# Optimization experiments

Hardware: AMD Instinct MI355X
Metric: run time of the kernel (lower is better)

Reference implementation:

```python
import jax, jax.numpy as jnp
import numpy as np

N, E, D_IN, H, D_OUT = 50000, 1600000, 256, 128, 64


def setup_inputs() -> dict:
    key = jax.random.key(0)
    ks = jax.random.split(key, 8)
    x = jax.random.normal(ks[0], (N, D_IN), dtype=jnp.float32)
    edge_index = jax.random.randint(ks[1], (2, E), 0, N, dtype=jnp.int64)
    W1 = jax.random.normal(ks[2], (D_IN, H), dtype=jnp.float32) / np.float32(np.sqrt(D_IN))
    b1 = jnp.zeros((H,), jnp.float32)
    W2 = jax.random.normal(ks[3], (H, H), dtype=jnp.float32) / np.float32(np.sqrt(H))
    b2 = jnp.zeros((H,), jnp.float32)
    W3 = jax.random.normal(ks[4], (H, D_OUT), dtype=jnp.float32) / np.float32(np.sqrt(H))
    b3 = jnp.zeros((D_OUT,), jnp.float32)
    return {"x": x, "W1": W1, "b1": b1, "W2": W2, "b2": b2, "W3": W3, "b3": b3,
            "edge_index": edge_index}


def reference(x, W1, b1, W2, b2, W3, b3, edge_index):
    n = x.shape[0]
    # GCN: add self-loops, symmetric normalization D^{-1/2}(A+I)D^{-1/2}
    loop = jnp.arange(n, dtype=edge_index.dtype)
    src = jnp.concatenate([edge_index[0], loop])
    dst = jnp.concatenate([edge_index[1], loop])
    deg = jax.ops.segment_sum(jnp.ones_like(dst, x.dtype), dst, num_segments=n)
    dinv = jnp.where(deg > 0, jax.lax.rsqrt(deg), 0.0).astype(x.dtype)
    norm = dinv[src] * dinv[dst]  # [E+N]

    def gcn_layer(h, W, b):
        h = h @ W                                   # [N, F_out]
        msg = norm[:, None] * h[src]                # gather + scale, [E+N, F_out]
        return jax.ops.segment_sum(msg, dst, num_segments=n) + b

    h = jax.nn.relu(gcn_layer(x, W1, b1))
    h = jax.nn.relu(gcn_layer(h, W2, b2))
    return gcn_layer(h, W3, b3)
```

## Files before the change

kernel.cpp:

```cpp
#include <hip/hip_runtime.h>


constexpr int DIN = 256;
constexpr int HID = 128;
constexpr int DOUT = 64;
constexpr int MAXB = 1024;
constexpr int BSH = 6;
constexpr int EPB = 8192;

typedef unsigned short ushort_t;
typedef unsigned int uint_t;
typedef __attribute__((ext_vector_type(8))) short bf16x8;
typedef __attribute__((ext_vector_type(4))) float f32x4;

__device__ inline ushort_t f2bf(float f) {
  uint_t u = __float_as_uint(f);
  u += 0x7FFF + ((u >> 16) & 1);
  return (ushort_t)(u >> 16);
}
__device__ inline float bf2f(ushort_t b) {
  return __uint_as_float(((uint_t)b) << 16);
}

template <int SH>
__device__ inline uint_t ldrow32(const ushort_t* __restrict__ t, int c, uint_t lb) {
  return *(const uint_t*)((const char*)t + ((((uint_t)c) << SH) | lb));
}
template <int SH>
__device__ inline ushort_t ldrow16(const ushort_t* __restrict__ t, int c, uint_t lb) {
  return *(const ushort_t*)((const char*)t + ((((uint_t)c) << SH) | lb));
}
__device__ inline float ldf32(const float* __restrict__ p, int c) {
  return *(const float*)((const char*)p + (((uint_t)c) << 2));
}


__device__ inline void wprep_one(const float* __restrict__ W, ushort_t* __restrict__ Bhi,
                                 ushort_t* __restrict__ Blo, int K, int F, int i) {
  int k = i / F, nn = i % F;
  int t = nn >> 4, s = k >> 5, q = (k >> 3) & 3, j = k & 7;
  int lane = q * 16 + (nn & 15);
  int KS = K >> 5;
  size_t idx = (((size_t)t * KS + s) * 64 + (size_t)lane) * 8 + j;
  float w = W[i];
  ushort_t h = f2bf(w);
  float r = w - bf2f(h);
  Bhi[idx] = h;
  Blo[idx] = f2bf(r);
}


__global__ __launch_bounds__(256) void initprep_kernel(
    int* __restrict__ bucket_total, int* __restrict__ done, int iblocks,
    const float* __restrict__ W1, ushort_t* __restrict__ W1hi, ushort_t* __restrict__ W1lo,
    const float* __restrict__ W2, ushort_t* __restrict__ W2hi, ushort_t* __restrict__ W2lo,
    const float* __restrict__ W3, ushort_t* __restrict__ W3hi, ushort_t* __restrict__ W3lo) {
  if ((int)blockIdx.x < iblocks) {
    int i = blockIdx.x * 256 + threadIdx.x;
    if (i < MAXB) bucket_total[i] = 0;
    if (i == 0) *done = 0;
  } else {
    int idx = ((int)blockIdx.x - iblocks) * 256 + threadIdx.x;
    constexpr int S1 = DIN * HID;
    constexpr int S2 = S1 + HID * HID;
    constexpr int S3 = S2 + HID * DOUT;
    if (idx < S1) wprep_one(W1, W1hi, W1lo, DIN, HID, idx);
    else if (idx < S2) wprep_one(W2, W2hi, W2lo, HID, HID, idx - S1);
    else if (idx < S3) wprep_one(W3, W3hi, W3lo, HID, DOUT, idx - S2);
  }
}


__global__ __launch_bounds__(256) void bin_kernel(const int* __restrict__ dst, int e,
    int nbuckets, int* __restrict__ bucket_total, int* __restrict__ block_base,
    int* __restrict__ bucket_base, int* __restrict__ done, int nbin) {
  __shared__ int h[MAXB];
  __shared__ int lastflag;
  int tid = threadIdx.x;
  for (int i = tid; i < nbuckets; i += 256) h[i] = 0;
  __syncthreads();
  int base = blockIdx.x * EPB;
  int end = min(base + EPB, e);
  for (int i = base + tid; i < end; i += 256) atomicAdd(&h[dst[i] >> BSH], 1);
  __syncthreads();
  for (int i = tid; i < nbuckets; i += 256) {
    int v = h[i];
    if (v) block_base[(size_t)blockIdx.x * nbuckets + i] = atomicAdd(&bucket_total[i], v);
  }
  __threadfence();
  __syncthreads();
  if (tid == 0) lastflag = (atomicAdd(done, 1) == nbin - 1) ? 1 : 0;
  __syncthreads();
  if (!lastflag) return;
  int a[4];
  int ls = 0;
#pragma unroll
  for (int k = 0; k < 4; ++k) {
    int idx = tid * 4 + k;
    a[k] = (idx < nbuckets) ? atomicAdd(&bucket_total[idx], 0) : 0;
    ls += a[k];
  }
  __syncthreads();
  h[tid] = ls;
  __syncthreads();
  for (int off = 1; off < 256; off <<= 1) {
    int u = (tid >= off) ? h[tid - off] : 0;
    __syncthreads();
    h[tid] += u;
    __syncthreads();
  }
  int run = h[tid] - ls;
#pragma unroll
  for (int k = 0; k < 4; ++k) {
    int idx = tid * 4 + k;
    if (idx < nbuckets) bucket_base[idx] = run;
    run += a[k];
  }
  if (tid == 255) bucket_base[nbuckets] = h[255];
}


template <int K, int F, bool SCALE>
__device__ inline void gemm_mfma_dev(const float* __restrict__ X,
    const ushort_t* __restrict__ Bhi, const ushort_t* __restrict__ Blo,
    const float* __restrict__ dinv, ushort_t* __restrict__ T, int n, int bid) {
  constexpr int NT = F / 16;
  constexpr int KS = K / 32;
  int wave = threadIdx.x >> 6;
  int lane = threadIdx.x & 63;
  int q = lane >> 4;
  int m = lane & 15;
  int arow = bid * 64 + wave * 16 + m;
  bool valid = arow < n;
  const float* xrow = X + (size_t)arow * K;

  f32x4 acc[NT];
#pragma unroll
  for (int t = 0; t < NT; ++t) acc[t] = (f32x4){0.f, 0.f, 0.f, 0.f};

  for (int s = 0; s < KS; ++s) {
    float av[8];
    if (valid) {
      float4 u0 = *(const float4*)(xrow + s * 32 + q * 8);
      float4 u1 = *(const float4*)(xrow + s * 32 + q * 8 + 4);
      av[0] = u0.x; av[1] = u0.y; av[2] = u0.z; av[3] = u0.w;
      av[4] = u1.x; av[5] = u1.y; av[6] = u1.z; av[7] = u1.w;
    } else {
#pragma unroll
      for (int j = 0; j < 8; ++j) av[j] = 0.f;
    }
    bf16x8 ahi, alo;
#pragma unroll
    for (int j = 0; j < 8; ++j) {
      ushort_t h = f2bf(av[j]);
      ahi[j] = (short)h;
      alo[j] = (short)f2bf(av[j] - bf2f(h));
    }
#pragma unroll
    for (int t = 0; t < NT; ++t) {
      size_t boff = (((size_t)t * KS + s) * 64 + (size_t)lane) * 8;
      bf16x8 bh = *(const bf16x8*)(Bhi + boff);
      bf16x8 bl = *(const bf16x8*)(Blo + boff);
      acc[t] = __builtin_amdgcn_mfma_f32_16x16x32_bf16(ahi, bh, acc[t], 0, 0, 0);
      acc[t] = __builtin_amdgcn_mfma_f32_16x16x32_bf16(alo, bh, acc[t], 0, 0, 0);
      acc[t] = __builtin_amdgcn_mfma_f32_16x16x32_bf16(ahi, bl, acc[t], 0, 0, 0);
    }
  }

  int orow_base = bid * 64 + wave * 16 + q * 4;
#pragma unroll
  for (int r = 0; r < 4; ++r) {
    int orow = orow_base + r;
    if (orow >= n) continue;
    float sc = SCALE ? dinv[orow] : 1.0f;
    ushort_t* trow = T + (size_t)orow * F + m;
#pragma unroll
    for (int t = 0; t < NT; ++t) trow[t * 16] = f2bf(sc * acc[t][r]);
  }
}


__global__ __launch_bounds__(256) void fusedA2_kernel(
    const float* __restrict__ X, const ushort_t* __restrict__ Bhi,
    const ushort_t* __restrict__ Blo, ushort_t* __restrict__ T, int n, int gblocks,
    const int* __restrict__ src, const int* __restrict__ dst,
    const int* __restrict__ bucket_base, const int* __restrict__ block_base,
    uint_t* __restrict__ binned, int e, int nbuckets) {
  if ((int)blockIdx.x < gblocks) {
    gemm_mfma_dev<DIN, HID, false>(X, Bhi, Blo, nullptr, T, n, blockIdx.x);
  } else {
    __shared__ int rkh[MAXB];
    __shared__ int cbase[MAXB];
    int tid = threadIdx.x;
    int blk = (int)blockIdx.x - gblocks;
    for (int i = tid; i < nbuckets; i += 256) {
      rkh[i] = 0;
      cbase[i] = bucket_base[i] + block_base[(size_t)blk * nbuckets + i];
    }
    __syncthreads();
    int base = blk * EPB;
    int end = min(base + EPB, e);
    for (int i = base + tid; i < end; i += 256) {
      int d = dst[i];
      int s = src[i];
      int b = d >> BSH;
      int r = atomicAdd(&rkh[b], 1);
      binned[cbase[b] + r] = ((uint_t)d << 16) | (uint_t)s;
    }
  }
}


__global__ __launch_bounds__(256) void csr_kernel(const uint_t* __restrict__ binned,
    const int* __restrict__ bucket_base, int n, int* __restrict__ row_start,
    int* __restrict__ deg, float* __restrict__ dinv, int* __restrict__ col) {
  __shared__ int cnt[64];
  __shared__ int rk[64];
  __shared__ int rs[64];
  __shared__ int ebs[2];
  int tid = threadIdx.x;
  int b = blockIdx.x;
  int node0 = b << BSH;
  if (tid < 64) { cnt[tid] = 0; rk[tid] = 0; }
  if (tid == 0) { ebs[0] = bucket_base[b]; ebs[1] = bucket_base[b + 1]; }
  __syncthreads();
  int ebase = ebs[0];
  int esz = ebs[1] - ebase;
  for (int i = tid; i < esz; i += 256)
    atomicAdd(&cnt[(int)(binned[ebase + i] >> 16) - node0], 1);
  __syncthreads();
  if (tid < 64) {
    int v = cnt[tid];
    int inc = v;
#pragma unroll
    for (int off = 1; off < 64; off <<= 1) {
      int u = __shfl_up(inc, off, 64);
      if (tid >= off) inc += u;
    }
    rs[tid] = inc - v;
    int node = node0 + tid;
    if (node < n) {
      deg[node] = v + 1;
      dinv[node] = rsqrtf((float)(v + 1));
      row_start[node] = ebase + (inc - v);
    }
  }
  __syncthreads();
  for (int i = tid; i < esz; i += 256) {
    uint_t p = binned[ebase + i];
    int l = (int)(p >> 16) - node0;
    int r = atomicAdd(&rk[l], 1);
    col[ebase + rs[l] + r] = (int)(p & 0xFFFFu);
  }
}


template <int FOUT, bool GD>
__global__ __launch_bounds__(256) void spmm_gemm_kernel(
    const ushort_t* __restrict__ t, const int* __restrict__ row_start,
    const int* __restrict__ deg, const int* __restrict__ col,
    const float* __restrict__ dinv, const float* __restrict__ bias,
    const ushort_t* __restrict__ Bhi, const ushort_t* __restrict__ Blo,
    ushort_t* __restrict__ Tout, int n) {
  constexpr int FIN = 128;
  constexpr int NPB = 8;
  constexpr int LDW = FIN + 4;
  __shared__ float agg[16][LDW];
  int wave = threadIdx.x >> 6;
  int lane = threadIdx.x & 63;
  int tid = threadIdx.x;
  int nb0 = (int)blockIdx.x * NPB;
  uint_t lb = (uint_t)lane << 2;

  {
    float* z = &agg[8][0];
    for (int i = tid; i < 8 * LDW; i += 256) z[i] = 0.f;
  }

  {
    int ln0 = wave * 2;
    int n0 = nb0 + ln0;
    int n1 = n0 + 1;
    bool h0 = n0 < n, h1 = n1 < n;
    int rs0 = h0 ? row_start[n0] : 0, e0 = h0 ? deg[n0] - 1 : 0;
    int rs1 = h1 ? row_start[n1] : 0, e1 = h1 ? deg[n1] - 1 : 0;
    float di0 = h0 ? dinv[n0] : 0.f;
    float di1 = h1 ? dinv[n1] : 0.f;
    float bx = bias[2 * lane], by = bias[2 * lane + 1];
    float ax0 = 0.f, ay0 = 0.f, ax1 = 0.f, ay1 = 0.f;
    if (h0) {
      uint_t s0 = ldrow32<8>(t, n0, lb);
      ax0 = bf2f((ushort_t)(s0 & 0xFFFF)); ay0 = bf2f((ushort_t)(s0 >> 16));
      if constexpr (GD) { ax0 *= di0; ay0 *= di0; }
    }
    if (h1) {
      uint_t s1 = ldrow32<8>(t, n1, lb);
      ax1 = bf2f((ushort_t)(s1 & 0xFFFF)); ay1 = bf2f((ushort_t)(s1 >> 16));
      if constexpr (GD) { ax1 *= di1; ay1 *= di1; }
    }
    int p0 = rs0, q0 = rs0 + e0;
    int p1 = rs1, q1 = rs1 + e1;
    while (p0 + 4 <= q0 && p1 + 4 <= q1) {
      int c[8];
      uint_t v[8];
      float dc[8];
#pragma unroll
      for (int j = 0; j < 4; ++j) { c[j] = col[p0 + j]; c[4 + j] = col[p1 + j]; }
#pragma unroll
      for (int j = 0; j < 8; ++j) {
        v[j] = ldrow32<8>(t, c[j], lb);
        if constexpr (GD) dc[j] = ldf32(dinv, c[j]);
      }
#pragma unroll
      for (int j = 0; j < 4; ++j) {
        if constexpr (GD) {
          ax0 = fmaf(dc[j], bf2f((ushort_t)(v[j] & 0xFFFF)), ax0);
          ay0 = fmaf(dc[j], bf2f((ushort_t)(v[j] >> 16)), ay0);
          ax1 = fmaf(dc[4 + j], bf2f((ushort_t)(v[4 + j] & 0xFFFF)), ax1);
          ay1 = fmaf(dc[4 + j], bf2f((ushort_t)(v[4 + j] >> 16)), ay1);
        } else {
          ax0 += bf2f((ushort_t)(v[j] & 0xFFFF));
          ay0 += bf2f((ushort_t)(v[j] >> 16));
          ax1 += bf2f((ushort_t)(v[4 + j] & 0xFFFF));
          ay1 += bf2f((ushort_t)(v[4 + j] >> 16));
        }
      }
      p0 += 4; p1 += 4;
    }
    for (; p0 + 4 <= q0; p0 += 4) {
      int c[4]; uint_t v[4]; float dc[4];
#pragma unroll
      for (int j = 0; j < 4; ++j) c[j] = col[p0 + j];
#pragma unroll
      for (int j = 0; j < 4; ++j) {
        v[j] = ldrow32<8>(t, c[j], lb);
        if constexpr (GD) dc[j] = ldf32(dinv, c[j]);
      }
#pragma unroll
      for (int j = 0; j < 4; ++j) {
        if constexpr (GD) {
          ax0 = fmaf(dc[j], bf2f((ushort_t)(v[j] & 0xFFFF)), ax0);
          ay0 = fmaf(dc[j], bf2f((ushort_t)(v[j] >> 16)), ay0);
        } else {
          ax0 += bf2f((ushort_t)(v[j] & 0xFFFF)); ay0 += bf2f((ushort_t)(v[j] >> 16));
        }
      }
    }
    for (; p0 < q0; ++p0) {
      int c = col[p0];
      uint_t v = ldrow32<8>(t, c, lb);
      if constexpr (GD) {
        float d = ldf32(dinv, c);
        ax0 = fmaf(d, bf2f((ushort_t)(v & 0xFFFF)), ax0);
        ay0 = fmaf(d, bf2f((ushort_t)(v >> 16)), ay0);
      } else {
        ax0 += bf2f((ushort_t)(v & 0xFFFF)); ay0 += bf2f((ushort_t)(v >> 16));
      }
    }
    for (; p1 + 4 <= q1; p1 += 4) {
      int c[4]; uint_t v[4]; float dc[4];
#pragma unroll
      for (int j = 0; j < 4; ++j) c[j] = col[p1 + j];
#pragma unroll
      for (int j = 0; j < 4; ++j) {
        v[j] = ldrow32<8>(t, c[j], lb);
        if constexpr (GD) dc[j] = ldf32(dinv, c[j]);
      }
#pragma unroll
      for (int j = 0; j < 4; ++j) {
        if constexpr (GD) {
          ax1 = fmaf(dc[j], bf2f((ushort_t)(v[j] & 0xFFFF)), ax1);
          ay1 = fmaf(dc[j], bf2f((ushort_t)(v[j] >> 16)), ay1);
        } else {
          ax1 += bf2f((ushort_t)(v[j] & 0xFFFF)); ay1 += bf2f((ushort_t)(v[j] >> 16));
        }
      }
    }
    for (; p1 < q1; ++p1) {
      int c = col[p1];
      uint_t v = ldrow32<8>(t, c, lb);
      if constexpr (GD) {
        float d = ldf32(dinv, c);
        ax1 = fmaf(d, bf2f((ushort_t)(v & 0xFFFF)), ax1);
        ay1 = fmaf(d, bf2f((ushort_t)(v >> 16)), ay1);
      } else {
        ax1 += bf2f((ushort_t)(v & 0xFFFF)); ay1 += bf2f((ushort_t)(v >> 16));
      }
    }
    float2 o0, o1;
    o0.x = h0 ? fmaxf(fmaf(di0, ax0, bx), 0.f) : 0.f;
    o0.y = h0 ? fmaxf(fmaf(di0, ay0, by), 0.f) : 0.f;
    o1.x = h1 ? fmaxf(fmaf(di1, ax1, bx), 0.f) : 0.f;
    o1.y = h1 ? fmaxf(fmaf(di1, ay1, by), 0.f) : 0.f;
    *(float2*)&agg[ln0][2 * lane] = o0;
    *(float2*)&agg[ln0 + 1][2 * lane] = o1;
  }
  __syncthreads();

  constexpr int NT = FOUT / 16;
  constexpr int KS = FIN / 32;
  constexpr int NTW = NT / 4;
  int q = lane >> 4, m = lane & 15;
  f32x4 acc[NTW];
#pragma unroll
  for (int tt = 0; tt < NTW; ++tt) acc[tt] = (f32x4){0.f, 0.f, 0.f, 0.f};
  const float* arow = &agg[m][0];
#pragma unroll
  for (int s = 0; s < KS; ++s) {
    float4 u0 = *(const float4*)(arow + s * 32 + q * 8);
    float4 u1 = *(const float4*)(arow + s * 32 + q * 8 + 4);
    float av[8];
    av[0] = u0.x; av[1] = u0.y; av[2] = u0.z; av[3] = u0.w;
    av[4] = u1.x; av[5] = u1.y; av[6] = u1.z; av[7] = u1.w;
    bf16x8 ahi, alo;
#pragma unroll
    for (int j = 0; j < 8; ++j) {
      ushort_t h = f2bf(av[j]);
      ahi[j] = (short)h;
      alo[j] = (short)f2bf(av[j] - bf2f(h));
    }
#pragma unroll
    for (int tt = 0; tt < NTW; ++tt) {
      int tg = wave * NTW + tt;
      size_t boff = (((size_t)tg * KS + s) * 64 + (size_t)lane) * 8;
      bf16x8 bh = *(const bf16x8*)(Bhi + boff);
      bf16x8 bl = *(const bf16x8*)(Blo + boff);
      acc[tt] = __builtin_amdgcn_mfma_f32_16x16x32_bf16(ahi, bh, acc[tt], 0, 0, 0);
      acc[tt] = __builtin_amdgcn_mfma_f32_16x16x32_bf16(alo, bh, acc[tt], 0, 0, 0);
      acc[tt] = __builtin_amdgcn_mfma_f32_16x16x32_bf16(ahi, bl, acc[tt], 0, 0, 0);
    }
  }
#pragma unroll
  for (int r = 0; r < 4; ++r) {
    int row = q * 4 + r;
    if (row >= NPB) continue;
    int orow = nb0 + row;
    if (orow >= n) continue;
    float sc = dinv[orow];
    ushort_t* trow = Tout + (size_t)orow * FOUT + m;
#pragma unroll
    for (int tt = 0; tt < NTW; ++tt)
      trow[(wave * NTW + tt) * 16] = f2bf(sc * acc[tt][r]);
  }
}


template <int F, bool RELU>
__global__ __launch_bounds__(256) void spmm_kernel(const ushort_t* __restrict__ t,
    const int* __restrict__ row_start, const int* __restrict__ deg,
    const int* __restrict__ col, const float* __restrict__ dinv,
    const float* __restrict__ bias, float* __restrict__ out, int n) {
  static_assert(F == 64, "final layer only");
  int gw = (int)((blockIdx.x * 256u + threadIdx.x) >> 6);
  int lane = threadIdx.x & 63;
  int n0 = gw * 2;
  int n1 = n0 + 1;
  if (n0 >= n) return;
  bool h1 = (n1 < n);
  int rs0 = row_start[n0], e0 = deg[n0] - 1;
  int rs1 = h1 ? row_start[n1] : 0, e1 = h1 ? (deg[n1] - 1) : 0;
  float di0 = dinv[n0];
  float di1 = h1 ? dinv[n1] : 0.f;
  uint_t lb = (uint_t)lane << 1;

  float a0 = bf2f(ldrow16<7>(t, n0, lb));
  float a1 = h1 ? bf2f(ldrow16<7>(t, n1, lb)) : 0.f;
  int p0 = rs0, q0 = rs0 + e0;
  int p1 = rs1, q1 = rs1 + e1;
  while (p0 + 4 <= q0 && p1 + 4 <= q1) {
    int c[8];
    ushort_t v[8];
#pragma unroll
    for (int j = 0; j < 4; ++j) { c[j] = col[p0 + j]; c[4 + j] = col[p1 + j]; }
#pragma unroll
    for (int j = 0; j < 8; ++j) v[j] = ldrow16<7>(t, c[j], lb);
#pragma unroll
    for (int j = 0; j < 4; ++j) { a0 += bf2f(v[j]); a1 += bf2f(v[4 + j]); }
    p0 += 4; p1 += 4;
  }
  for (; p0 + 4 <= q0; p0 += 4) {
    int c[4]; ushort_t v[4];
#pragma unroll
    for (int j = 0; j < 4; ++j) c[j] = col[p0 + j];
#pragma unroll
    for (int j = 0; j < 4; ++j) v[j] = ldrow16<7>(t, c[j], lb);
#pragma unroll
    for (int j = 0; j < 4; ++j) a0 += bf2f(v[j]);
  }
  for (; p0 < q0; ++p0) a0 += bf2f(ldrow16<7>(t, col[p0], lb));
  for (; p1 + 4 <= q1; p1 += 4) {
    int c[4]; ushort_t v[4];
#pragma unroll
    for (int j = 0; j < 4; ++j) c[j] = col[p1 + j];
#pragma unroll
    for (int j = 0; j < 4; ++j) v[j] = ldrow16<7>(t, c[j], lb);
#pragma unroll
    for (int j = 0; j < 4; ++j) a1 += bf2f(v[j]);
  }
  for (; p1 < q1; ++p1) a1 += bf2f(ldrow16<7>(t, col[p1], lb));
  float b = bias[lane];
  a0 = fmaf(di0, a0, b);
  if constexpr (RELU) a0 = fmaxf(a0, 0.f);
  out[(size_t)n0 * F + lane] = a0;
  if (h1) {
    a1 = fmaf(di1, a1, b);
    if constexpr (RELU) a1 = fmaxf(a1, 0.f);
    out[(size_t)n1 * F + lane] = a1;
  }
}


extern "C" void kernel_launch(void* const* d_in, const int* in_sizes, int n_in,
                              void* d_out, int out_size, void* d_ws, size_t ws_size,
                              hipStream_t stream) {
  const float* x  = (const float*)d_in[0];
  const float* W1 = (const float*)d_in[1];
  const float* b1 = (const float*)d_in[2];
  const float* W2 = (const float*)d_in[3];
  const float* b2 = (const float*)d_in[4];
  const float* W3 = (const float*)d_in[5];
  const float* b3 = (const float*)d_in[6];
  const int* ei   = (const int*)d_in[7];

  int n = in_sizes[0] / DIN;
  int e = in_sizes[7] / 2;
  const int* src = ei;
  const int* dst = ei + e;

  char* ws = (char*)d_ws;
  size_t off = 0;
  auto alloc = [&](size_t bytes) -> void* {
    off = (off + 255) & ~(size_t)255;
    void* p = ws + off;
    off += bytes;
    return p;
  };
  int nbuckets = (n + 63) >> BSH;
  int nbin = (e + EPB - 1) / EPB;

  int*      bucket_total = (int*)alloc((size_t)MAXB * 4);
  int*      bucket_base  = (int*)alloc((size_t)(MAXB + 1) * 4);
  int*      done         = (int*)alloc(256);
  int*      block_base   = (int*)alloc((size_t)nbin * nbuckets * 4);
  uint_t*   binned       = (uint_t*)alloc((size_t)e * 4);
  int*      deg          = (int*)alloc((size_t)n * 4);
  float*    dinv         = (float*)alloc((size_t)n * 4);
  int*      row_start    = (int*)alloc((size_t)n * 4);
  int*      col          = (int*)alloc((size_t)e * 4);
  ushort_t* Ta           = (ushort_t*)alloc((size_t)n * HID * 2);
  ushort_t* Tb           = (ushort_t*)alloc((size_t)n * HID * 2);
  ushort_t* W1hi         = (ushort_t*)alloc((size_t)DIN * HID * 2);
  ushort_t* W1lo         = (ushort_t*)alloc((size_t)DIN * HID * 2);
  ushort_t* W2hi         = (ushort_t*)alloc((size_t)HID * HID * 2);
  ushort_t* W2lo         = (ushort_t*)alloc((size_t)HID * HID * 2);
  ushort_t* W3hi         = (ushort_t*)alloc((size_t)HID * DOUT * 2);
  ushort_t* W3lo         = (ushort_t*)alloc((size_t)HID * DOUT * 2);
  (void)ws_size;

  int gemm_blocks = (n + 63) / 64;
  int sg_blocks = (n + 7) / 8;
  int nwaves = (n + 1) / 2;
  int spmm_blocks = (nwaves + 3) / 4;
  constexpr int WPREP_TOTAL = DIN * HID + HID * HID + HID * DOUT;
  int wblocks = (WPREP_TOTAL + 255) / 256;
  int iblocks = MAXB / 256;

  initprep_kernel<<<iblocks + wblocks, 256, 0, stream>>>(
      bucket_total, done, iblocks,
      W1, W1hi, W1lo, W2, W2hi, W2lo, W3, W3hi, W3lo);
  bin_kernel<<<nbin, 256, 0, stream>>>(dst, e, nbuckets, bucket_total, block_base,
                                       bucket_base, done, nbin);
  fusedA2_kernel<<<gemm_blocks + nbin, 256, 0, stream>>>(
      x, W1hi, W1lo, Ta, n, gemm_blocks,
      src, dst, bucket_base, block_base, binned, e, nbuckets);
  csr_kernel<<<nbuckets, 256, 0, stream>>>(binned, bucket_base, n, row_start, deg, dinv, col);

  spmm_gemm_kernel<HID, true><<<sg_blocks, 256, 0, stream>>>(
      Ta, row_start, deg, col, dinv, b1, W2hi, W2lo, Tb, n);
  spmm_gemm_kernel<DOUT, false><<<sg_blocks, 256, 0, stream>>>(
      Tb, row_start, deg, col, dinv, b2, W3hi, W3lo, Ta, n);
  spmm_kernel<DOUT, false><<<spmm_blocks, 256, 0, stream>>>(
      Ta, row_start, deg, col, dinv, b3, (float*)d_out, n);
}
```

Baseline: 361.8 us.

## Split bucket scan into own kernel and remap final SpMM to half-wave per node

Removes the last-block-done atomic counter and threadfence from the binning kernel and moves the bucket prefix scan into a separate single-block kernel. The final 64-wide SpMM now gives each half-wave one node, with each lane loading two bf16 features as a 32-bit word and writing float2 outputs. Both nodes in a wave step through the longer edge list together with predicated loads. The changes cut global synchronisation and per-lane load count, at the price of one extra launch and lanes that sit idle when the two nodes have unequal degrees.

```diff
diff --git a/kernel.cpp b/kernel.cpp
--- a/kernel.cpp
+++ b/kernel.cpp
@@ -25,10 +25,6 @@
 template <int SH>
 __device__ inline uint_t ldrow32(const ushort_t* __restrict__ t, int c, uint_t lb) {
   return *(const uint_t*)((const char*)t + ((((uint_t)c) << SH) | lb));
-}
-template <int SH>
-__device__ inline ushort_t ldrow16(const ushort_t* __restrict__ t, int c, uint_t lb) {
-  return *(const ushort_t*)((const char*)t + ((((uint_t)c) << SH) | lb));
 }
 __device__ inline float ldf32(const float* __restrict__ p, int c) {
   return *(const float*)((const char*)p + (((uint_t)c) << 2));
@@ -51,14 +47,13 @@
 
 
 __global__ __launch_bounds__(256) void initprep_kernel(
-    int* __restrict__ bucket_total, int* __restrict__ done, int iblocks,
+    int* __restrict__ bucket_total, int iblocks,
     const float* __restrict__ W1, ushort_t* __restrict__ W1hi, ushort_t* __restrict__ W1lo,
     const float* __restrict__ W2, ushort_t* __restrict__ W2hi, ushort_t* __restrict__ W2lo,
     const float* __restrict__ W3, ushort_t* __restrict__ W3hi, ushort_t* __restrict__ W3lo) {
   if ((int)blockIdx.x < iblocks) {
     int i = blockIdx.x * 256 + threadIdx.x;
     if (i < MAXB) bucket_total[i] = 0;
-    if (i == 0) *done = 0;
   } else {
     int idx = ((int)blockIdx.x - iblocks) * 256 + threadIdx.x;
     constexpr int S1 = DIN * HID;
@@ -72,10 +67,8 @@
 
 
 __global__ __launch_bounds__(256) void bin_kernel(const int* __restrict__ dst, int e,
-    int nbuckets, int* __restrict__ bucket_total, int* __restrict__ block_base,
-    int* __restrict__ bucket_base, int* __restrict__ done, int nbin) {
+    int nbuckets, int* __restrict__ bucket_total, int* __restrict__ block_base) {
   __shared__ int h[MAXB];
-  __shared__ int lastflag;
   int tid = threadIdx.x;
   for (int i = tid; i < nbuckets; i += 256) h[i] = 0;
   __syncthreads();
@@ -87,36 +80,37 @@
     int v = h[i];
     if (v) block_base[(size_t)blockIdx.x * nbuckets + i] = atomicAdd(&bucket_total[i], v);
   }
-  __threadfence();
-  __syncthreads();
-  if (tid == 0) lastflag = (atomicAdd(done, 1) == nbin - 1) ? 1 : 0;
-  __syncthreads();
-  if (!lastflag) return;
+}
+
+
+__global__ __launch_bounds__(256) void scan_buckets_kernel(const int* __restrict__ total,
+    int* __restrict__ base, int nb) {
+  __shared__ int sums[256];
+  int t = threadIdx.x;
   int a[4];
   int ls = 0;
 #pragma unroll
   for (int k = 0; k < 4; ++k) {
-    int idx = tid * 4 + k;
-    a[k] = (idx < nbuckets) ? atomicAdd(&bucket_total[idx], 0) : 0;
+    int idx = t * 4 + k;
+    a[k] = (idx < nb) ? total[idx] : 0;
     ls += a[k];
   }
-  __syncthreads();
-  h[tid] = ls;
+  sums[t] = ls;
   __syncthreads();
   for (int off = 1; off < 256; off <<= 1) {
-    int u = (tid >= off) ? h[tid - off] : 0;
+    int u = (t >= off) ? sums[t - off] : 0;
     __syncthreads();
-    h[tid] += u;
+    sums[t] += u;
     __syncthreads();
   }
-  int run = h[tid] - ls;
+  int run = sums[t] - ls;
 #pragma unroll
   for (int k = 0; k < 4; ++k) {
-    int idx = tid * 4 + k;
-    if (idx < nbuckets) bucket_base[idx] = run;
+    int idx = t * 4 + k;
+    if (idx < nb) base[idx] = run;
     run += a[k];
   }
-  if (tid == 255) bucket_base[nbuckets] = h[255];
+  if (t == 255) base[nb] = sums[255];
 }
 
 
@@ -445,67 +439,55 @@
 }
 
 
-template <int F, bool RELU>
-__global__ __launch_bounds__(256) void spmm_kernel(const ushort_t* __restrict__ t,
+__global__ __launch_bounds__(256) void spmm64_kernel(const ushort_t* __restrict__ t,
     const int* __restrict__ row_start, const int* __restrict__ deg,
     const int* __restrict__ col, const float* __restrict__ dinv,
     const float* __restrict__ bias, float* __restrict__ out, int n) {
-  static_assert(F == 64, "final layer only");
   int gw = (int)((blockIdx.x * 256u + threadIdx.x) >> 6);
   int lane = threadIdx.x & 63;
+  int half = lane >> 5;
+  int hl = lane & 31;
   int n0 = gw * 2;
-  int n1 = n0 + 1;
   if (n0 >= n) return;
-  bool h1 = (n1 < n);
-  int rs0 = row_start[n0], e0 = deg[n0] - 1;
-  int rs1 = h1 ? row_start[n1] : 0, e1 = h1 ? (deg[n1] - 1) : 0;
-  float di0 = dinv[n0];
-  float di1 = h1 ? dinv[n1] : 0.f;
-  uint_t lb = (uint_t)lane << 1;
-
-  float a0 = bf2f(ldrow16<7>(t, n0, lb));
-  float a1 = h1 ? bf2f(ldrow16<7>(t, n1, lb)) : 0.f;
-  int p0 = rs0, q0 = rs0 + e0;
-  int p1 = rs1, q1 = rs1 + e1;
-  while (p0 + 4 <= q0 && p1 + 4 <= q1) {
-    int c[8];
-    ushort_t v[8];
-#pragma unroll
-    for (int j = 0; j < 4; ++j) { c[j] = col[p0 + j]; c[4 + j] = col[p1 + j]; }
-#pragma unroll
-    for (int j = 0; j < 8; ++j) v[j] = ldrow16<7>(t, c[j], lb);
-#pragma unroll
-    for (int j = 0; j < 4; ++j) { a0 += bf2f(v[j]); a1 += bf2f(v[4 + j]); }
-    p0 += 4; p1 += 4;
-  }
-  for (; p0 + 4 <= q0; p0 += 4) {
-    int c[4]; ushort_t v[4];
-#pragma unroll
-    for (int j = 0; j < 4; ++j) c[j] = col[p0 + j];
-#pragma unroll
-    for (int j = 0; j < 4; ++j) v[j] = ldrow16<7>(t, c[j], lb);
-#pragma unroll
-    for (int j = 0; j < 4; ++j) a0 += bf2f(v[j]);
-  }
-  for (; p0 < q0; ++p0) a0 += bf2f(ldrow16<7>(t, col[p0], lb));
-  for (; p1 + 4 <= q1; p1 += 4) {
-    int c[4]; ushort_t v[4];
-#pragma unroll
-    for (int j = 0; j < 4; ++j) c[j] = col[p1 + j];
-#pragma unroll
-    for (int j = 0; j < 4; ++j) v[j] = ldrow16<7>(t, c[j], lb);
-#pragma unroll
-    for (int j = 0; j < 4; ++j) a1 += bf2f(v[j]);
-  }
-  for (; p1 < q1; ++p1) a1 += bf2f(ldrow16<7>(t, col[p1], lb));
-  float b = bias[lane];
-  a0 = fmaf(di0, a0, b);
-  if constexpr (RELU) a0 = fmaxf(a0, 0.f);
-  out[(size_t)n0 * F + lane] = a0;
-  if (h1) {
-    a1 = fmaf(di1, a1, b);
-    if constexpr (RELU) a1 = fmaxf(a1, 0.f);
-    out[(size_t)n1 * F + lane] = a1;
+  int node = n0 + half;
+  bool valid = node < n;
+  int vnode = valid ? node : n0;
+  int rs = row_start[vnode];
+  int e  = valid ? (deg[vnode] - 1) : 0;
+  float di = dinv[vnode];
+  uint_t lb = (uint_t)hl << 2;
+
+  uint_t su = ldrow32<7>(t, vnode, lb);
+  float ax = bf2f((ushort_t)(su & 0xFFFF));
+  float ay = bf2f((ushort_t)(su >> 16));
+
+  int emax = max(e, __shfl_xor(e, 32));
+  for (int k = 0; k < emax; k += 4) {
+    int c[4];
+    uint_t v[4];
+#pragma unroll
+    for (int j = 0; j < 4; ++j) {
+      int on = (k + j) < e;
+      c[j] = col[on ? (rs + k + j) : 0];
+    }
+#pragma unroll
+    for (int j = 0; j < 4; ++j) v[j] = ldrow32<7>(t, c[j], lb);
+#pragma unroll
+    for (int j = 0; j < 4; ++j) {
+      if ((k + j) < e) {
+        ax += bf2f((ushort_t)(v[j] & 0xFFFF));
+        ay += bf2f((ushort_t)(v[j] >> 16));
+      }
+    }
+  }
+  if (valid) {
+    float bx = bias[2 * hl], by = bias[2 * hl + 1];
+    ax = fmaf(di, ax, bx);
+    ay = fmaf(di, ay, by);
+    float2 o;
+    o.x = ax;
+    o.y = ay;
+    *(float2*)(out + (size_t)node * DOUT + 2 * hl) = o;
   }
 }
 
@@ -540,7 +522,6 @@
 
   int*      bucket_total = (int*)alloc((size_t)MAXB * 4);
   int*      bucket_base  = (int*)alloc((size_t)(MAXB + 1) * 4);
-  int*      done         = (int*)alloc(256);
   int*      block_base   = (int*)alloc((size_t)nbin * nbuckets * 4);
   uint_t*   binned       = (uint_t*)alloc((size_t)e * 4);
   int*      deg          = (int*)alloc((size_t)n * 4);
@@ -566,10 +547,10 @@
   int iblocks = MAXB / 256;
 
   initprep_kernel<<<iblocks + wblocks, 256, 0, stream>>>(
-      bucket_total, done, iblocks,
+      bucket_total, iblocks,
       W1, W1hi, W1lo, W2, W2hi, W2lo, W3, W3hi, W3lo);
-  bin_kernel<<<nbin, 256, 0, stream>>>(dst, e, nbuckets, bucket_total, block_base,
-                                       bucket_base, done, nbin);
+  bin_kernel<<<nbin, 256, 0, stream>>>(dst, e, nbuckets, bucket_total, block_base);
+  scan_buckets_kernel<<<1, 256, 0, stream>>>(bucket_total, bucket_base, nbuckets);
   fusedA2_kernel<<<gemm_blocks + nbin, 256, 0, stream>>>(
       x, W1hi, W1lo, Ta, n, gemm_blocks,
       src, dst, bucket_base, block_base, binned, e, nbuckets);
@@ -579,6 +560,6 @@
       Ta, row_start, deg, col, dinv, b1, W2hi, W2lo, Tb, n);
   spmm_gemm_kernel<DOUT, false><<<sg_blocks, 256, 0, stream>>>(
       Tb, row_start, deg, col, dinv, b2, W3hi, W3lo, Ta, n);
-  spmm_kernel<DOUT, false><<<spmm_blocks, 256, 0, stream>>>(
+  spmm64_kernel<<<spmm_blocks, 256, 0, stream>>>(
       Ta, row_start, deg, col, dinv, b3, (float*)d_out, n);
 }
```

New measurement: 356.8 us. About the same (-1.4%).
